# Kernel tuning notes

Hardware: AMD Instinct MI355X
Metric: run time of the kernel (lower is better)

## Reference

```python
import jax, jax.numpy as jnp
import numpy as np
from functools import reduce

N = 16          # total qubits
N_SQC = 4       # shadow-circuit qubits
BATCH = 512
DIM = 2 ** N    # 65536
CX = jnp.complex64


def multi_kron(mats):
    return reduce(jnp.kron, mats)


def ry(t):
    c = jnp.cos(t / 2).astype(CX)
    s = jnp.sin(t / 2).astype(CX)
    return jnp.stack([jnp.stack([c, -s]), jnp.stack([s, c])])


def rz(t):
    e = jnp.exp(-0.5j * t.astype(CX))
    z = jnp.zeros((), CX)
    return jnp.stack([jnp.stack([e, z]), jnp.stack([z, jnp.conj(e)])])


def yzy_layer(params, n):
    # per qubit i: apply Ry(p[3i]), Rz(p[3i+1]), Ry(p[3i+2]) -> u_i = Ry@Rz@Ry
    us = [ry(params[3 * i + 2]) @ rz(params[3 * i + 1]) @ ry(params[3 * i])
          for i in range(n)]
    return multi_kron(us)


def cnot(n, c, t):
    I = jnp.eye(2, dtype=CX)
    X = jnp.array([[0, 1], [1, 0]], dtype=CX)
    P0 = jnp.array([[1, 0], [0, 0]], dtype=CX)
    P1 = jnp.array([[0, 0], [0, 1]], dtype=CX)
    ops0 = [I] * n; ops0[c] = P0
    ops1 = [I] * n; ops1[c] = P1; ops1[t] = X
    return multi_kron(ops0) + multi_kron(ops1)


def ring_of_cnot(n):
    U = jnp.eye(2 ** n, dtype=CX)
    for i in range(n):  # CNOT(i, (i+1)%n) applied in order
        U = cnot(n, i, (i + 1) % n) @ U
    return U


def build_circuit(weight, n):
    # BasicEntangleLayer(repeat=2): [YZYLayer, ring_of_cnot] x 2, then final YZYLayer
    repeat = 2
    U = jnp.eye(2 ** n, dtype=CX)
    ring = ring_of_cnot(n)
    for r in range(repeat):
        U = yzy_layer(weight[3 * n * r:3 * n * (r + 1)], n) @ U
        U = ring @ U
    U = yzy_layer(weight[3 * n * repeat:3 * n * (repeat + 1)], n) @ U
    return U


def setup_inputs() -> dict:
    key = jax.random.key(0)
    k1, k2 = jax.random.split(key)
    vector_batch = jax.random.normal(k1, (BATCH, DIM), dtype=jnp.float32)
    weight = jax.random.uniform(k2, (9 * N_SQC,), dtype=jnp.float32,
                                minval=0.0, maxval=2.0 * np.pi)
    return {"vector_batch": vector_batch, "weight": weight}


def reference(vector_batch, weight):
    # row-wise L2 normalization + amplitude encoding (pad to 2**N), cast complex
    norm = jnp.sqrt(jnp.sum(vector_batch * vector_batch, axis=1, keepdims=True))
    state = (vector_batch / norm).astype(CX)
    state = jnp.pad(state, ((0, 0), (0, DIM - state.shape[1])))  # (B, 2^N)

    U = build_circuit(weight, N_SQC)                 # (2^n_sqc, 2^n_sqc)
    X = jnp.array([[0, 1], [1, 0]], dtype=CX)
    M = multi_kron([X] * N_SQC)                      # PauliX^{(x)n_sqc}
    T = U.conj().T @ M @ U                           # effective observable

    m = 2 ** N_SQC
    outs = []
    for start in range(N - N_SQC + 1):
        left = 2 ** start
        right = DIM // (left * m)
        # trace(rho * (I (x) T (x) I)) == <s| I (x) T (x) I |s>
        s = state.reshape(BATCH, left, m, right)
        y = jnp.einsum('ij,bajd->baid', T, s)
        o = jnp.einsum('baid,baid->b', jnp.conj(s), y).real
        outs.append(o)
    return jnp.stack(outs, axis=1).astype(jnp.float32)  # (B, N - n_sqc + 1)
```

## Files before the change

kernel.cpp:

```cpp
#include <hip/hip_runtime.h>
#include <math.h>


typedef _Float16 f16x8 __attribute__((ext_vector_type(8)));
typedef float f32x4 __attribute__((ext_vector_type(4)));
#define MFMAH(a, b, c) __builtin_amdgcn_mfma_f32_16x16x32_f16((a), (b), (c), 0, 0, 0)

union H4 { _Float16 h[4]; uint2 q; };
union Frag { _Float16 h[8]; f16x8 v; uint2 q[2]; unsigned int w[4]; };

__device__ __forceinline__ int swz(int g) { return g ^ (g >> 5); }

__device__ __forceinline__ float wave_sum(float x) {
    #pragma unroll
    for (int off = 32; off > 0; off >>= 1) x += __shfl_down(x, off, 64);
    return x;
}

using c2 = float2;
__device__ __forceinline__ c2 cmul(c2 a, c2 b) {
    return make_float2(a.x * b.x - a.y * b.y, a.x * b.y + a.y * b.x);
}
__device__ __forceinline__ c2 cadd(c2 a, c2 b) { return make_float2(a.x + b.x, a.y + b.y); }

__device__ __forceinline__ c2 kelem(const c2 u[4][2][2], int i, int j) {
    c2 p = cmul(u[0][(i >> 3) & 1][(j >> 3) & 1], u[1][(i >> 2) & 1][(j >> 2) & 1]);
    p = cmul(p, u[2][(i >> 1) & 1][(j >> 1) & 1]);
    p = cmul(p, u[3][i & 1][j & 1]);
    return p;
}
__device__ __forceinline__ int fperm(int x) {
    int b3 = (x >> 3) & 1, b2 = (x >> 2) & 1, b1 = (x >> 1) & 1, b0 = x & 1;
    b2 ^= b3; b1 ^= b2; b0 ^= b1; b3 ^= b0;
    return (b3 << 3) | (b2 << 2) | (b1 << 1) | b0;
}

__global__ __launch_bounds__(256) void setup_kernel(const float* __restrict__ weight,
                                                    float* __restrict__ ws) {
    __shared__ c2 ush[3][4][2][2];
    __shared__ c2 A[256], B[256];
    const int t = threadIdx.x;

    if (t < 12) {
        const int r = t / 4, q = t % 4;
        const float a = weight[12 * r + 3 * q + 0];
        const float b = weight[12 * r + 3 * q + 1];
        const float c = weight[12 * r + 3 * q + 2];
        const float ca = cosf(0.5f * a), sa = sinf(0.5f * a);
        const float cc = cosf(0.5f * c), sc = sinf(0.5f * c);
        const c2 e = make_float2(cosf(0.5f * b), -sinf(0.5f * b));
        const c2 eb = make_float2(e.x, -e.y);
        ush[r][q][0][0] = make_float2(cc * ca * e.x - sc * sa * eb.x, cc * ca * e.y - sc * sa * eb.y);
        ush[r][q][0][1] = make_float2(-cc * sa * e.x - sc * ca * eb.x, -cc * sa * e.y - sc * ca * eb.y);
        ush[r][q][1][0] = make_float2(sc * ca * e.x + cc * sa * eb.x, sc * ca * e.y + cc * sa * eb.y);
        ush[r][q][1][1] = make_float2(-sc * sa * e.x + cc * ca * eb.x, -sc * sa * e.y + cc * ca * eb.y);
    }
    __syncthreads();

    const int i = t >> 4, j = t & 15;
    A[t] = kelem(ush[0], i, j);
    __syncthreads();
    B[fperm(i) * 16 + j] = A[t];
    __syncthreads();
    {
        c2 acc = make_float2(0.f, 0.f);
        #pragma unroll
        for (int k = 0; k < 16; ++k) acc = cadd(acc, cmul(kelem(ush[1], i, k), B[k * 16 + j]));
        __syncthreads();
        A[t] = acc;
    }
    __syncthreads();
    B[fperm(i) * 16 + j] = A[t];
    __syncthreads();
    {
        c2 acc = make_float2(0.f, 0.f);
        #pragma unroll
        for (int k = 0; k < 16; ++k) acc = cadd(acc, cmul(kelem(ush[2], i, k), B[k * 16 + j]));
        __syncthreads();
        A[t] = acc;
    }
    __syncthreads();
    {
        float wr = 0.f;
        #pragma unroll
        for (int k = 0; k < 16; ++k) {
            const c2 a = A[k * 16 + i];
            const c2 b = A[(k ^ 15) * 16 + j];
            wr += a.x * b.x + a.y * b.y;
        }
        ws[t] = wr;
    }
    for (int z = t; z < 512 * 14; z += 256) ws[256 + z] = 0.f;
}

__global__ __launch_bounds__(256, 6) void main_kernel(const float* __restrict__ v,
                                                      const float* __restrict__ ws,
                                                      float* __restrict__ accg) {
    __shared__ unsigned short sh16[8192];
    __shared__ float Wl[256];
    const int t = threadIdx.x;
    const int l = t & 63, wv = t >> 6;
    const int i = l & 15, h = l >> 4;
    Wl[t] = ws[t];

    if (blockIdx.x < 4096) {
        const int row = blockIdx.x >> 3, seg = blockIdx.x & 7;
        const float4* b4 = (const float4*)(v + ((size_t)row << 16) + (seg << 13));

        float ss = 0.f;
        #pragma unroll
        for (int m = 0; m < 8; ++m) {
            const float4 d = b4[m * 256 + t];
            ss = fmaf(d.x, d.x, ss); ss = fmaf(d.y, d.y, ss);
            ss = fmaf(d.z, d.z, ss); ss = fmaf(d.w, d.w, ss);
            H4 p;
            p.h[0] = (_Float16)d.x; p.h[1] = (_Float16)d.y;
            p.h[2] = (_Float16)d.z; p.h[3] = (_Float16)d.w;
            const int e0 = (m * 256 + t) * 4;
            const int idx = (swz(e0 >> 3) << 3) + (e0 & 7);
            *(uint2*)&sh16[idx] = p.q;
        }
        {
            const float s2 = wave_sum(ss);
            if (l == 0) atomicAdd(&accg[row * 14 + 13], s2);
        }
        __syncthreads();

        int f = 36 * wv;
        const int fend = f + 36;
        while (f < fend) {
            const int sidx = f >> 4;
            const int s = 3 + sidx;
            const int bnd = (sidx + 1) << 4;
            const int cstop = (bnd < fend) ? bnd : fend;
            const int lst = 12 - s;
            f32x4 acc = {0.f, 0.f, 0.f, 0.f};
            if (s <= 9) {
                #pragma unroll 4
                for (int ff = f; ff < cstop; ++ff) {
                    const int g0 = 32 * (ff & 15) + 8 * h;
                    const int a = g0 >> lst, d0 = g0 & ((1 << lst) - 1);
                    const int e0 = (a << (lst + 4)) + (i << lst) + d0;
                    const f16x8 fh = *(const f16x8*)&sh16[swz(e0 >> 3) << 3];
                    acc = MFMAH(fh, fh, acc);
                }
            } else if (s == 10) {
                #pragma unroll 4
                for (int ff = f; ff < cstop; ++ff) {
                    const int a0 = 8 * (ff & 15) + 2 * h;
                    const int ea = a0 * 64 + 4 * i;
                    const int eb = ea + 64;
                    Frag fr;
                    fr.q[0] = *(const uint2*)&sh16[(swz(ea >> 3) << 3) + (ea & 7)];
                    fr.q[1] = *(const uint2*)&sh16[(swz(eb >> 3) << 3) + (eb & 7)];
                    acc = MFMAH(fr.v, fr.v, acc);
                }
            } else {
                #pragma unroll 4
                for (int ff = f; ff < cstop; ++ff) {
                    const int a0 = 16 * (ff & 15) + 4 * h;
                    Frag fr;
                    #pragma unroll
                    for (int p = 0; p < 4; ++p) {
                        const int e = (a0 + p) * 32 + 2 * i;
                        fr.w[p] = *(const unsigned int*)&sh16[(swz(e >> 3) << 3) + (e & 7)];
                    }
                    acc = MFMAH(fr.v, fr.v, acc);
                }
            }
            const float4 wr = *(const float4*)&Wl[(i << 4) + (h << 2)];
            float q = wr.x * acc[0] + wr.y * acc[1] + wr.z * acc[2] + wr.w * acc[3];
            q = wave_sum(q);
            if (l == 0) atomicAdd(&accg[row * 14 + s], q);
            f = cstop;
        }
    } else {
        const int bi = blockIdx.x - 4096;
        const int row = bi >> 3;
        const int c0 = (bi & 7) << 6;
        const float* bp = v + ((size_t)row << 16) + c0 + l;

        #pragma unroll
        for (int m = 0; m < 8; ++m) {
            const int u0 = 32 * wv + 4 * m;
            H4 p;
            p.h[0] = (_Float16)bp[(u0 + 0) * 512];
            p.h[1] = (_Float16)bp[(u0 + 1) * 512];
            p.h[2] = (_Float16)bp[(u0 + 2) * 512];
            p.h[3] = (_Float16)bp[(u0 + 3) * 512];
            *(uint2*)&sh16[l * 128 + (u0 ^ (8 * (l & 15)))] = p.q;
        }
        __syncthreads();

        f32x4 acc = {0.f, 0.f, 0.f, 0.f};
        int s;
        if (wv == 0) {
            s = 0;
            #pragma unroll 4
            for (int cc = 0; cc < 16; ++cc) {
                const int cl = 4 * cc + h;
                const f16x8 fh = *(const f16x8*)&sh16[cl * 128 + ((8 * i) ^ (8 * (cl & 15)))];
                acc = MFMAH(fh, fh, acc);
            }
        } else if (wv == 1) {
            s = 1;
            #pragma unroll 4
            for (int cc = 0; cc < 16; ++cc) {
                const int cl = 4 * cc + h;
                const int k = 8 * (cl & 15);
                Frag fr;
                fr.q[0] = *(const uint2*)&sh16[cl * 128 + ((4 * i) ^ k)];
                fr.q[1] = *(const uint2*)&sh16[cl * 128 + ((64 + 4 * i) ^ k)];
                acc = MFMAH(fr.v, fr.v, acc);
            }
        } else if (wv == 2) {
            s = 2;
            #pragma unroll 4
            for (int cc = 0; cc < 16; ++cc) {
                const int cl = 4 * cc + h;
                const int k = 8 * (cl & 15);
                Frag fr;
                #pragma unroll
                for (int p = 0; p < 4; ++p)
                    fr.w[p] = *(const unsigned int*)&sh16[cl * 128 + ((2 * i + 32 * p) ^ k)];
                acc = MFMAH(fr.v, fr.v, acc);
            }
        } else {
            s = 12;
            #pragma unroll 4
            for (int cc = 0; cc < 16; ++cc) {
                const int k0 = 32 * cc + 8 * h;
                const int cg = k0 >> 7, u0 = k0 & 127;
                const int col = 16 * cg + i;
                const f16x8 fh = *(const f16x8*)&sh16[col * 128 + (u0 ^ (8 * i))];
                acc = MFMAH(fh, fh, acc);
            }
        }
        const float4 wr = *(const float4*)&Wl[(i << 4) + (h << 2)];
        float q = wr.x * acc[0] + wr.y * acc[1] + wr.z * acc[2] + wr.w * acc[3];
        q = wave_sum(q);
        if (l == 0) atomicAdd(&accg[row * 14 + s], q);
    }
}

__global__ __launch_bounds__(256) void finalize_kernel(const float* __restrict__ acc,
                                                       float* __restrict__ out) {
    const int idx = blockIdx.x * 256 + threadIdx.x;
    if (idx < 512 * 13) {
        const int row = idx / 13, s = idx % 13;
        out[idx] = acc[row * 14 + s] / acc[row * 14 + 13];
    }
}

extern "C" void kernel_launch(void* const* d_in, const int* in_sizes, int n_in,
                              void* d_out, int out_size, void* d_ws, size_t ws_size,
                              hipStream_t stream) {
    const float* vb = (const float*)d_in[0];
    const float* wt = (const float*)d_in[1];
    float* out = (float*)d_out;
    float* ws = (float*)d_ws;
    float* acc = ws + 256;

    setup_kernel<<<1, 256, 0, stream>>>(wt, ws);
    main_kernel<<<8192, 256, 0, stream>>>(vb, ws, acc);
    finalize_kernel<<<26, 256, 0, stream>>>(acc, out);
}
```

Baseline: 208.9 us.

## Fuse adjacent shift pairs into 32x32 MFMA and rebalance per-wave work

Adjacent observable positions (3/4, 5/6, 7/8) are now computed from a single 32x32x16 MFMA Gram matrix per wave, with two weighted contractions taken from its 16x16 sub-blocks instead of separate 16x16 MFMA passes. The remaining shifts are split evenly across waves with fully unrolled loops, and in the transposed blocks part of the s=2 work moves from wave 2 to wave 1. The goal is fewer MFMA issues and LDS loads per block, in exchange for more accumulator registers, which is reflected in lowering the launch-bounds occupancy hint from 6 to 5.

```diff
diff --git a/kernel.cpp b/kernel.cpp
--- a/kernel.cpp
+++ b/kernel.cpp
@@ -4,7 +4,9 @@
 
 typedef _Float16 f16x8 __attribute__((ext_vector_type(8)));
 typedef float f32x4 __attribute__((ext_vector_type(4)));
+typedef float f32x16 __attribute__((ext_vector_type(16)));
 #define MFMAH(a, b, c) __builtin_amdgcn_mfma_f32_16x16x32_f16((a), (b), (c), 0, 0, 0)
+#define MFMA32(a, b, c) __builtin_amdgcn_mfma_f32_32x32x16_f16((a), (b), (c), 0, 0, 0)
 
 union H4 { _Float16 h[4]; uint2 q; };
 union Frag { _Float16 h[8]; f16x8 v; uint2 q[2]; unsigned int w[4]; };
@@ -93,7 +95,99 @@
     for (int z = t; z < 512 * 14; z += 256) ws[256 + z] = 0.f;
 }
 
-__global__ __launch_bounds__(256, 6) void main_kernel(const float* __restrict__ v,
+
+__device__ __forceinline__ void contract16(const float* __restrict__ Wl, const f32x4& acc,
+                                           int i, int h, int l, float* dst) {
+    const float4 wr = *(const float4*)&Wl[(i << 4) + (h << 2)];
+    float q = wr.x * acc[0] + wr.y * acc[1] + wr.z * acc[2] + wr.w * acc[3];
+    q = wave_sum(q);
+    if (l == 0) atomicAdd(dst, q);
+}
+
+template <int S>
+__device__ __forceinline__ void pair_unit(const unsigned short* __restrict__ sh16,
+                                          const float* __restrict__ Wl,
+                                          int l, float* accrow) {
+    const int Jp = l & 31, h2 = l >> 5;
+    f32x16 acc = {0.f, 0.f, 0.f, 0.f, 0.f, 0.f, 0.f, 0.f,
+                  0.f, 0.f, 0.f, 0.f, 0.f, 0.f, 0.f, 0.f};
+    #pragma unroll
+    for (int cc = 0; cc < 16; ++cc) {
+        int e0;
+        if (S == 3)      e0 = (Jp << 8) + (cc << 4) + (h2 << 3);
+        else if (S == 5) e0 = ((cc >> 2) << 11) + (Jp << 6) + ((cc & 3) << 4) + (h2 << 3);
+        else             e0 = (cc << 9) + (Jp << 4) + (h2 << 3);
+        const f16x8 f = *(const f16x8*)&sh16[swz(e0 >> 3) << 3];
+        acc = MFMA32(f, f, acc);
+    }
+    float qa = 0.f, qb = 0.f;
+    #pragma unroll
+    for (int r2 = 0; r2 < 8; ++r2) {
+        const int r = 2 * r2;
+        const int J = (r & 3) + 8 * (r >> 2) + 4 * h2;
+        const float w = Wl[((J >> 1) << 4) + (Jp >> 1)];
+        qa += w * ((Jp & 1) ? acc[r + 1] : acc[r]);
+    }
+    #pragma unroll
+    for (int r = 0; r < 8; ++r) {
+        const int J = (r & 3) + 8 * (r >> 2) + 4 * h2;
+        const float w = Wl[((J & 15) << 4) + (Jp & 15)];
+        qb += w * ((Jp & 16) ? acc[r + 8] : acc[r]);
+    }
+    qa = wave_sum(qa);
+    qb = wave_sum(qb);
+    if (l == 0) { atomicAdd(&accrow[S], qa); atomicAdd(&accrow[S + 1], qb); }
+}
+
+__device__ __forceinline__ void unit9(const unsigned short* __restrict__ sh16,
+                                      const float* __restrict__ Wl,
+                                      int i, int h, int l, float* accrow) {
+    f32x4 acc = {0.f, 0.f, 0.f, 0.f};
+    #pragma unroll
+    for (int cc = 0; cc < 16; ++cc) {
+        const int e0 = ((4 * cc + h) << 7) + (i << 3);
+        const f16x8 f = *(const f16x8*)&sh16[swz(e0 >> 3) << 3];
+        acc = MFMAH(f, f, acc);
+    }
+    contract16(Wl, acc, i, h, l, &accrow[9]);
+}
+
+__device__ __forceinline__ void unit10(const unsigned short* __restrict__ sh16,
+                                       const float* __restrict__ Wl,
+                                       int i, int h, int l, int c0, int c1, float* accrow) {
+    f32x4 acc = {0.f, 0.f, 0.f, 0.f};
+    #pragma unroll
+    for (int cc = c0; cc < c1; ++cc) {
+        const int a0 = 8 * cc + 2 * h;
+        const int ea = a0 * 64 + 4 * i;
+        const int eb = ea + 64;
+        Frag fr;
+        fr.q[0] = *(const uint2*)&sh16[(swz(ea >> 3) << 3) + (ea & 7)];
+        fr.q[1] = *(const uint2*)&sh16[(swz(eb >> 3) << 3) + (eb & 7)];
+        acc = MFMAH(fr.v, fr.v, acc);
+    }
+    contract16(Wl, acc, i, h, l, &accrow[10]);
+}
+
+__device__ __forceinline__ void unit11(const unsigned short* __restrict__ sh16,
+                                       const float* __restrict__ Wl,
+                                       int i, int h, int l, int c0, int c1, float* accrow) {
+    f32x4 acc = {0.f, 0.f, 0.f, 0.f};
+    #pragma unroll
+    for (int cc = c0; cc < c1; ++cc) {
+        Frag fr;
+        #pragma unroll
+        for (int p = 0; p < 4; ++p) {
+            const int ap = 16 * cc + 4 * h + p;
+            const int e = ap * 32 + 2 * i;
+            fr.w[p] = *(const unsigned int*)&sh16[(swz(e >> 3) << 3) + (e & 7)];
+        }
+        acc = MFMAH(fr.v, fr.v, acc);
+    }
+    contract16(Wl, acc, i, h, l, &accrow[11]);
+}
+
+__global__ __launch_bounds__(256, 5) void main_kernel(const float* __restrict__ v,
                                                       const float* __restrict__ ws,
                                                       float* __restrict__ accg) {
     __shared__ unsigned short sh16[8192];
@@ -106,6 +200,7 @@
     if (blockIdx.x < 4096) {
         const int row = blockIdx.x >> 3, seg = blockIdx.x & 7;
         const float4* b4 = (const float4*)(v + ((size_t)row << 16) + (seg << 13));
+        float* accrow = &accg[row * 14];
 
         float ss = 0.f;
         #pragma unroll
@@ -122,63 +217,29 @@
         }
         {
             const float s2 = wave_sum(ss);
-            if (l == 0) atomicAdd(&accg[row * 14 + 13], s2);
+            if (l == 0) atomicAdd(&accrow[13], s2);
         }
         __syncthreads();
 
-        int f = 36 * wv;
-        const int fend = f + 36;
-        while (f < fend) {
-            const int sidx = f >> 4;
-            const int s = 3 + sidx;
-            const int bnd = (sidx + 1) << 4;
-            const int cstop = (bnd < fend) ? bnd : fend;
-            const int lst = 12 - s;
-            f32x4 acc = {0.f, 0.f, 0.f, 0.f};
-            if (s <= 9) {
-                #pragma unroll 4
-                for (int ff = f; ff < cstop; ++ff) {
-                    const int g0 = 32 * (ff & 15) + 8 * h;
-                    const int a = g0 >> lst, d0 = g0 & ((1 << lst) - 1);
-                    const int e0 = (a << (lst + 4)) + (i << lst) + d0;
-                    const f16x8 fh = *(const f16x8*)&sh16[swz(e0 >> 3) << 3];
-                    acc = MFMAH(fh, fh, acc);
-                }
-            } else if (s == 10) {
-                #pragma unroll 4
-                for (int ff = f; ff < cstop; ++ff) {
-                    const int a0 = 8 * (ff & 15) + 2 * h;
-                    const int ea = a0 * 64 + 4 * i;
-                    const int eb = ea + 64;
-                    Frag fr;
-                    fr.q[0] = *(const uint2*)&sh16[(swz(ea >> 3) << 3) + (ea & 7)];
-                    fr.q[1] = *(const uint2*)&sh16[(swz(eb >> 3) << 3) + (eb & 7)];
-                    acc = MFMAH(fr.v, fr.v, acc);
-                }
-            } else {
-                #pragma unroll 4
-                for (int ff = f; ff < cstop; ++ff) {
-                    const int a0 = 16 * (ff & 15) + 4 * h;
-                    Frag fr;
-                    #pragma unroll
-                    for (int p = 0; p < 4; ++p) {
-                        const int e = (a0 + p) * 32 + 2 * i;
-                        fr.w[p] = *(const unsigned int*)&sh16[(swz(e >> 3) << 3) + (e & 7)];
-                    }
-                    acc = MFMAH(fr.v, fr.v, acc);
-                }
-            }
-            const float4 wr = *(const float4*)&Wl[(i << 4) + (h << 2)];
-            float q = wr.x * acc[0] + wr.y * acc[1] + wr.z * acc[2] + wr.w * acc[3];
-            q = wave_sum(q);
-            if (l == 0) atomicAdd(&accg[row * 14 + s], q);
-            f = cstop;
+        if (wv == 0) {
+            pair_unit<3>(sh16, Wl, l, accrow);
+            unit10(sh16, Wl, i, h, l, 0, 8, accrow);
+        } else if (wv == 1) {
+            pair_unit<5>(sh16, Wl, l, accrow);
+            unit10(sh16, Wl, i, h, l, 8, 16, accrow);
+        } else if (wv == 2) {
+            pair_unit<7>(sh16, Wl, l, accrow);
+            unit11(sh16, Wl, i, h, l, 0, 8, accrow);
+        } else {
+            unit9(sh16, Wl, i, h, l, accrow);
+            unit11(sh16, Wl, i, h, l, 8, 16, accrow);
         }
     } else {
         const int bi = blockIdx.x - 4096;
         const int row = bi >> 3;
         const int c0 = (bi & 7) << 6;
         const float* bp = v + ((size_t)row << 16) + c0 + l;
+        float* accrow = &accg[row * 14];
 
         #pragma unroll
         for (int m = 0; m < 8; ++m) {
@@ -192,31 +253,47 @@
         }
         __syncthreads();
 
-        f32x4 acc = {0.f, 0.f, 0.f, 0.f};
-        int s;
         if (wv == 0) {
-            s = 0;
-            #pragma unroll 4
+            f32x4 acc = {0.f, 0.f, 0.f, 0.f};
+            #pragma unroll
             for (int cc = 0; cc < 16; ++cc) {
                 const int cl = 4 * cc + h;
-                const f16x8 fh = *(const f16x8*)&sh16[cl * 128 + ((8 * i) ^ (8 * (cl & 15)))];
-                acc = MFMAH(fh, fh, acc);
-            }
+                const f16x8 f = *(const f16x8*)&sh16[cl * 128 + ((8 * i) ^ (8 * (cl & 15)))];
+                acc = MFMAH(f, f, acc);
+            }
+            contract16(Wl, acc, i, h, l, &accrow[0]);
         } else if (wv == 1) {
-            s = 1;
-            #pragma unroll 4
-            for (int cc = 0; cc < 16; ++cc) {
-                const int cl = 4 * cc + h;
-                const int k = 8 * (cl & 15);
-                Frag fr;
-                fr.q[0] = *(const uint2*)&sh16[cl * 128 + ((4 * i) ^ k)];
-                fr.q[1] = *(const uint2*)&sh16[cl * 128 + ((64 + 4 * i) ^ k)];
-                acc = MFMAH(fr.v, fr.v, acc);
+            {
+                f32x4 acc = {0.f, 0.f, 0.f, 0.f};
+                #pragma unroll
+                for (int cc = 0; cc < 16; ++cc) {
+                    const int cl = 4 * cc + h;
+                    const int k = 8 * (cl & 15);
+                    Frag fr;
+                    fr.q[0] = *(const uint2*)&sh16[cl * 128 + ((4 * i) ^ k)];
+                    fr.q[1] = *(const uint2*)&sh16[cl * 128 + ((64 + 4 * i) ^ k)];
+                    acc = MFMAH(fr.v, fr.v, acc);
+                }
+                contract16(Wl, acc, i, h, l, &accrow[1]);
+            }
+            {
+                f32x4 acc = {0.f, 0.f, 0.f, 0.f};
+                #pragma unroll
+                for (int cc = 12; cc < 16; ++cc) {
+                    const int cl = 4 * cc + h;
+                    const int k = 8 * (cl & 15);
+                    Frag fr;
+                    #pragma unroll
+                    for (int p = 0; p < 4; ++p)
+                        fr.w[p] = *(const unsigned int*)&sh16[cl * 128 + ((2 * i + 32 * p) ^ k)];
+                    acc = MFMAH(fr.v, fr.v, acc);
+                }
+                contract16(Wl, acc, i, h, l, &accrow[2]);
             }
         } else if (wv == 2) {
-            s = 2;
-            #pragma unroll 4
-            for (int cc = 0; cc < 16; ++cc) {
+            f32x4 acc = {0.f, 0.f, 0.f, 0.f};
+            #pragma unroll
+            for (int cc = 0; cc < 12; ++cc) {
                 const int cl = 4 * cc + h;
                 const int k = 8 * (cl & 15);
                 Frag fr;
@@ -225,21 +302,19 @@
                     fr.w[p] = *(const unsigned int*)&sh16[cl * 128 + ((2 * i + 32 * p) ^ k)];
                 acc = MFMAH(fr.v, fr.v, acc);
             }
+            contract16(Wl, acc, i, h, l, &accrow[2]);
         } else {
-            s = 12;
-            #pragma unroll 4
+            f32x4 acc = {0.f, 0.f, 0.f, 0.f};
+            #pragma unroll
             for (int cc = 0; cc < 16; ++cc) {
                 const int k0 = 32 * cc + 8 * h;
                 const int cg = k0 >> 7, u0 = k0 & 127;
                 const int col = 16 * cg + i;
-                const f16x8 fh = *(const f16x8*)&sh16[col * 128 + (u0 ^ (8 * i))];
-                acc = MFMAH(fh, fh, acc);
-            }
-        }
-        const float4 wr = *(const float4*)&Wl[(i << 4) + (h << 2)];
-        float q = wr.x * acc[0] + wr.y * acc[1] + wr.z * acc[2] + wr.w * acc[3];
-        q = wave_sum(q);
-        if (l == 0) atomicAdd(&accg[row * 14 + s], q);
+                const f16x8 f = *(const f16x8*)&sh16[col * 128 + (u0 ^ (8 * i))];
+                acc = MFMAH(f, f, acc);
+            }
+            contract16(Wl, acc, i, h, l, &accrow[12]);
+        }
     }
 }
 
```

Measured after the change: 209.7 us. No clear change (+0.4%).
